# Optimization experiments

Hardware: AMD Instinct MI355X
Metric: run time of the kernel (lower is better)

The kernel has to match this reference:

```python
import jax, jax.numpy as jnp
import numpy as np


def setup_inputs() -> dict:
    key = jax.random.key(0)
    k1, k2, k3, k4, k5 = jax.random.split(key, 5)
    M, K, N, E = 16384, 2048, 5632, 8  # total_tokens, d_model, expert ffn dim, num_experts
    a = jax.random.normal(k1, (M, K), jnp.float32) * 0.1          # fp8-valued activations (simulated in f32)
    b = jax.random.normal(k2, (E, N, K), jnp.float32) * 0.05      # column-major expert weights [E, N, K]
    scale_a = jax.random.uniform(k3, (M, 1), jnp.float32, 0.5, 1.5)   # per-token dequant scale
    scale_b = jax.random.uniform(k4, (E, 1), jnp.float32, 0.5, 1.5)   # per-expert dequant scale
    cuts = jnp.sort(jax.random.randint(k5, (E - 1,), 0, M)).astype(jnp.int32)
    seg_indptr = jnp.concatenate([jnp.zeros(1, jnp.int32), cuts, jnp.full((1,), M, jnp.int32)])
    return {"a": a, "b": b, "scale_a": scale_a, "scale_b": scale_b,
            "seg_indptr": seg_indptr, "batch_size": E}


def reference(a, b, scale_a, scale_b, seg_indptr, batch_size):
    # Grouped GEMM: for expert e, rows seg_indptr[e]:seg_indptr[e+1] of `a` are
    # multiplied by b[e]^T (b is column-major [E, N, K]).
    M = a.shape[0]
    E = b.shape[0]
    group_sizes = jnp.diff(seg_indptr).astype(jnp.int32)           # [E]
    out = jax.lax.ragged_dot(a, jnp.swapaxes(b, 1, 2), group_sizes)  # [M, N]
    # fp8 w8a8 dequant: per-token scale_a, per-expert scale_b gathered per token
    eid = jnp.clip(jnp.searchsorted(seg_indptr, jnp.arange(M), side='right') - 1, 0, E - 1)
    return out * scale_a * scale_b[eid]
```

## Files before the change

kernel.cpp:

```cpp
#include <hip/hip_runtime.h>


#define BK 64
#define NTILES 32
#define BM 256
#define BN 256
#define KDIM 2048

typedef __attribute__((ext_vector_type(4))) float f32x4;
typedef __attribute__((ext_vector_type(4))) unsigned int u32x4;
using frag_ab = __attribute__((ext_vector_type(8))) short;
using frag_cd = __attribute__((ext_vector_type(4))) float;

__device__ __forceinline__ unsigned int pack_bf2(float x, float y) {
  unsigned int ux = __float_as_uint(x);
  unsigned int uy = __float_as_uint(y);
  ux += 0x7fffu + ((ux >> 16) & 1u);
  uy += 0x7fffu + ((uy >> 16) & 1u);
  return (ux >> 16) | (uy & 0xffff0000u);
}

__device__ __forceinline__ void gload_lds16(const void* g, void* lds) {
  __builtin_amdgcn_global_load_lds(
      (const __attribute__((address_space(1))) unsigned int*)g,
      (__attribute__((address_space(3))) unsigned int*)lds, 16, 0, 0);
}

__global__ __launch_bounds__(256)
void convert_kernel(const float* __restrict__ A, const float* __restrict__ B,
                    unsigned short* __restrict__ wa, unsigned short* __restrict__ wb) {
  constexpr long long NA = 16384LL * 2048;
  constexpr long long NB = 8LL * 5632 * 2048;
  constexpr long long NA8 = NA / 8;
  constexpr long long NTOT = (NA + NB) / 8;
  for (long long c = (long long)blockIdx.x * 256 + threadIdx.x; c < NTOT;
       c += (long long)gridDim.x * 256) {
    const float* src;
    unsigned short* dst;
    long long off;
    if (c < NA8) { src = A; dst = wa; off = c * 8; }
    else         { src = B; dst = wb; off = (c - NA8) * 8; }
    f32x4 v0 = *(const f32x4*)(src + off);
    f32x4 v1 = *(const f32x4*)(src + off + 4);
    u32x4 o;
    o[0] = pack_bf2(v0[0], v0[1]);
    o[1] = pack_bf2(v0[2], v0[3]);
    o[2] = pack_bf2(v1[0], v1[1]);
    o[3] = pack_bf2(v1[2], v1[3]);
    *(u32x4*)(dst + off) = o;
  }
}

__global__ __launch_bounds__(512, 2)
void ggemm_q(const unsigned short* __restrict__ A,
             const unsigned short* __restrict__ B,
             const float* __restrict__ sa,
             const float* __restrict__ sb,
             const int* __restrict__ seg,
             float* __restrict__ C) {
  constexpr int M = 16384, N = 5632, E = 8;
  constexpr int NTC = N / BN;
  const int nwg = (M / BM) * NTC;

  int bid = blockIdx.x;
  int sid = (bid & 7) * (nwg >> 3) + (bid >> 3);
  int mt = sid / NTC, nt = sid % NTC;
  int m0 = mt * BM, n0 = nt * BN;

  int tid = threadIdx.x, lane = tid & 63, w = tid >> 6;
  int l16 = lane & 15, lhi = lane >> 4;
  int rw = (w & 1) * 64;
  int cw = (w >> 1) * 32;

  __shared__ unsigned short lds[2][2][2][8192];

  int c7 = l16 & 7;
  int x0 = (lhi ^ c7) * 8;
  int x1 = ((4 | lhi) ^ c7) * 8;
  int offA = (rw + l16) * 64;
  int offB = (cw + l16) * 64;
  int srow = lane >> 3;
  int scol = ((lane & 7) ^ srow) * 8;

  const unsigned short* gA = A + (size_t)(m0 + w * 16 + srow) * KDIM + scol;

  frag_ab af[2][4], bf0[2][2], bf1[2][2];

  for (int e = 0; e < E; ++e) {
    int rlo = max(m0, seg[e]);
    int rhi = min(m0 + BM, seg[e + 1]);
    if (rlo >= rhi) continue;
    const unsigned short* gB =
        B + (size_t)e * N * KDIM + (size_t)(n0 + w * 16 + srow) * KDIM + scol;

    frag_cd acc[4][4][2];
#pragma unroll
    for (int qi = 0; qi < 4; ++qi)
#pragma unroll
      for (int f = 0; f < 4; ++f)
#pragma unroll
        for (int g = 0; g < 2; ++g) acc[qi][f][g] = (frag_cd){0.f, 0.f, 0.f, 0.f};

    auto stA = [&](int buf, int half, int t) {
#pragma unroll
      for (int i = 0; i < 2; ++i)
        gload_lds16(gA + (size_t)(half * 128 + i * 8) * KDIM + t * BK,
                    &lds[buf][0][half][(w * 16 + i * 8) * 64]);
    };
    auto stB = [&](int buf, int half, int t) {
#pragma unroll
      for (int i = 0; i < 2; ++i)
        gload_lds16(gB + (size_t)(half * 128 + i * 8) * KDIM + t * BK,
                    &lds[buf][1][half][(w * 16 + i * 8) * 64]);
    };
    auto rdAf = [&](int buf, int half) {
      const unsigned short* p = &lds[buf][0][half][0];
#pragma unroll
      for (int f = 0; f < 4; ++f) {
        af[0][f] = *(const frag_ab*)(p + offA + f * 1024 + x0);
        af[1][f] = *(const frag_ab*)(p + offA + f * 1024 + x1);
      }
    };
    auto rdBf = [&](int buf, int half, frag_ab (&bf)[2][2]) {
      const unsigned short* p = &lds[buf][1][half][0];
#pragma unroll
      for (int g = 0; g < 2; ++g) {
        bf[0][g] = *(const frag_ab*)(p + offB + g * 1024 + x0);
        bf[1][g] = *(const frag_ab*)(p + offB + g * 1024 + x1);
      }
    };
    auto mfma16 = [&](int qi, frag_ab (&bf)[2][2]) {
      __builtin_amdgcn_s_setprio(1);
#pragma unroll
      for (int f = 0; f < 4; ++f)
#pragma unroll
        for (int g = 0; g < 2; ++g)
#pragma unroll
          for (int ks = 0; ks < 2; ++ks)
            acc[qi][f][g] = __builtin_amdgcn_mfma_f32_16x16x32_bf16(
                af[ks][f], bf[ks][g], acc[qi][f][g], 0, 0, 0);
      __builtin_amdgcn_s_setprio(0);
    };

    stA(0, 0, 0); stB(0, 0, 0); stB(0, 1, 0); stA(0, 1, 0);
    stA(1, 0, 1); stB(1, 0, 1); stB(1, 1, 1); stA(1, 1, 1);
    asm volatile("s_waitcnt vmcnt(8)" ::: "memory");
    __builtin_amdgcn_s_barrier();

    auto tile_body = [&](int t, int buf) {
      bool st = (t + 2 < NTILES);
      rdAf(buf, 0);
      rdBf(buf, 0, bf0);
      __builtin_amdgcn_s_barrier();
      mfma16(0, bf0);
      rdBf(buf, 1, bf1);
      if (st) { stA(buf, 0, t + 2); stB(buf, 0, t + 2); }
      __builtin_amdgcn_s_barrier();
      mfma16(1, bf1);
      rdAf(buf, 1);
      if (st) stB(buf, 1, t + 2);
      __builtin_amdgcn_s_barrier();
      mfma16(2, bf1);
      if (st) stA(buf, 1, t + 2);
      if (t < NTILES - 2) {
        asm volatile("s_waitcnt vmcnt(8)" ::: "memory");
      } else if (t == NTILES - 2) {
        asm volatile("s_waitcnt vmcnt(0)" ::: "memory");
      }
      __builtin_amdgcn_s_barrier();
      mfma16(3, bf0);
    };

    for (int t2 = 0; t2 < NTILES; t2 += 2) {
      tile_body(t2, 0);
      tile_body(t2 + 1, 1);
    }

    const int QMAP[4] = {0, 2, 3, 1};
    float sbe = sb[e];
#pragma unroll
    for (int qi = 0; qi < 4; ++qi) {
      int q = QMAP[qi];
      int rbase = m0 + (q & 1) * 128 + rw;
      int cbase = n0 + (q >> 1) * 128 + cw;
#pragma unroll
      for (int f = 0; f < 4; ++f) {
#pragma unroll
        for (int r = 0; r < 4; ++r) {
          int grow = rbase + f * 16 + lhi * 4 + r;
          if (grow >= rlo && grow < rhi) {
            float s = sa[grow] * sbe;
            float* Crow = C + (size_t)grow * N + cbase;
#pragma unroll
            for (int g = 0; g < 2; ++g)
              Crow[g * 16 + l16] = acc[qi][f][g][r] * s;
          }
        }
      }
    }
  }
}

extern "C" void kernel_launch(void* const* d_in, const int* in_sizes, int n_in,
                              void* d_out, int out_size, void* d_ws, size_t ws_size,
                              hipStream_t stream) {
  const float* a = (const float*)d_in[0];
  const float* b = (const float*)d_in[1];
  const float* sa = (const float*)d_in[2];
  const float* sb = (const float*)d_in[3];
  const int* seg = (const int*)d_in[4];
  float* out = (float*)d_out;

  constexpr size_t NA = 16384ULL * 2048;
  unsigned short* wa = (unsigned short*)d_ws;
  unsigned short* wb = wa + NA;

  hipLaunchKernelGGL(convert_kernel, dim3(2048), dim3(256), 0, stream, a, b, wa, wb);
  hipLaunchKernelGGL(ggemm_q, dim3((16384 / BM) * (5632 / BN)), dim3(512), 0, stream,
                     wa, wb, sa, sb, seg, out);
}
```

Before: 757.6 us.

## Restructure GEMM warp tiling to 128x64 per wave with new LDS pipeline

Changes each wave's output tile from four 64x32 quadrant pieces to one contiguous 128x64 block, holding eight A fragments and four B fragments per k-step. The per-tile schedule is rewritten to split the MFMA work into four 4x2 sub-blocks, interleaved with global-to-LDS prefetches and explicit lgkmcnt/vmcnt waits. The aim is more reuse of A and B fragments read from LDS, fewer LDS reads per MFMA, and a simpler epilogue. In exchange it raises register pressure through larger fragment arrays and adds more barriers, which could hurt occupancy at two workgroups per CU.

```diff
diff --git a/kernel.cpp b/kernel.cpp
--- a/kernel.cpp
+++ b/kernel.cpp
@@ -52,7 +52,7 @@
 }
 
 __global__ __launch_bounds__(512, 2)
-void ggemm_q(const unsigned short* __restrict__ A,
+void ggemm_t(const unsigned short* __restrict__ A,
              const unsigned short* __restrict__ B,
              const float* __restrict__ sa,
              const float* __restrict__ sb,
@@ -69,22 +69,26 @@
 
   int tid = threadIdx.x, lane = tid & 63, w = tid >> 6;
   int l16 = lane & 15, lhi = lane >> 4;
-  int rw = (w & 1) * 64;
-  int cw = (w >> 1) * 32;
-
-  __shared__ unsigned short lds[2][2][2][8192];
+  int wrow = (w >> 2) * 128;
+  int wcol = (w & 3) * 64;
+
+  __shared__ unsigned short Alds[2][256 * 64];
+  __shared__ unsigned short Blds[2][256 * 64];
 
   int c7 = l16 & 7;
-  int x0 = (lhi ^ c7) * 8;
-  int x1 = ((4 | lhi) ^ c7) * 8;
-  int offA = (rw + l16) * 64;
-  int offB = (cw + l16) * 64;
+  int x0 = ((0 + lhi) ^ c7) * 8;
+  int x1 = ((4 + lhi) ^ c7) * 8;
+  int offA[8], offB[4];
+#pragma unroll
+  for (int f = 0; f < 8; ++f) offA[f] = (wrow + f * 16 + l16) * 64;
+#pragma unroll
+  for (int g = 0; g < 4; ++g) offB[g] = (wcol + g * 16 + l16) * 64;
+
   int srow = lane >> 3;
   int scol = ((lane & 7) ^ srow) * 8;
-
   const unsigned short* gA = A + (size_t)(m0 + w * 16 + srow) * KDIM + scol;
 
-  frag_ab af[2][4], bf0[2][2], bf1[2][2];
+  frag_ab af[2][8], bf0[2][2], bf1[2][2];
 
   for (int e = 0; e < E; ++e) {
     int rlo = max(m0, seg[e]);
@@ -93,108 +97,101 @@
     const unsigned short* gB =
         B + (size_t)e * N * KDIM + (size_t)(n0 + w * 16 + srow) * KDIM + scol;
 
-    frag_cd acc[4][4][2];
-#pragma unroll
-    for (int qi = 0; qi < 4; ++qi)
-#pragma unroll
-      for (int f = 0; f < 4; ++f)
-#pragma unroll
-        for (int g = 0; g < 2; ++g) acc[qi][f][g] = (frag_cd){0.f, 0.f, 0.f, 0.f};
-
-    auto stA = [&](int buf, int half, int t) {
+    frag_cd acc[8][4];
+#pragma unroll
+    for (int f = 0; f < 8; ++f)
+#pragma unroll
+      for (int g = 0; g < 4; ++g) acc[f][g] = (frag_cd){0.f, 0.f, 0.f, 0.f};
+
+    auto stA = [&](int b, int h, int t) {
 #pragma unroll
       for (int i = 0; i < 2; ++i)
-        gload_lds16(gA + (size_t)(half * 128 + i * 8) * KDIM + t * BK,
-                    &lds[buf][0][half][(w * 16 + i * 8) * 64]);
-    };
-    auto stB = [&](int buf, int half, int t) {
+        gload_lds16(gA + (size_t)(h * 128 + i * 8) * KDIM + t * BK,
+                    &Alds[b][(h * 128 + w * 16 + i * 8) * 64]);
+    };
+    auto stB = [&](int b, int h, int t) {
 #pragma unroll
       for (int i = 0; i < 2; ++i)
-        gload_lds16(gB + (size_t)(half * 128 + i * 8) * KDIM + t * BK,
-                    &lds[buf][1][half][(w * 16 + i * 8) * 64]);
-    };
-    auto rdAf = [&](int buf, int half) {
-      const unsigned short* p = &lds[buf][0][half][0];
-#pragma unroll
-      for (int f = 0; f < 4; ++f) {
-        af[0][f] = *(const frag_ab*)(p + offA + f * 1024 + x0);
-        af[1][f] = *(const frag_ab*)(p + offA + f * 1024 + x1);
-      }
-    };
-    auto rdBf = [&](int buf, int half, frag_ab (&bf)[2][2]) {
-      const unsigned short* p = &lds[buf][1][half][0];
-#pragma unroll
-      for (int g = 0; g < 2; ++g) {
-        bf[0][g] = *(const frag_ab*)(p + offB + g * 1024 + x0);
-        bf[1][g] = *(const frag_ab*)(p + offB + g * 1024 + x1);
-      }
-    };
-    auto mfma16 = [&](int qi, frag_ab (&bf)[2][2]) {
+        gload_lds16(gB + (size_t)(h * 128 + i * 8) * KDIM + t * BK,
+                    &Blds[b][(h * 128 + w * 16 + i * 8) * 64]);
+    };
+    auto mfma16 = [&](int f0, int g0, frag_ab (&bf)[2][2]) {
       __builtin_amdgcn_s_setprio(1);
 #pragma unroll
-      for (int f = 0; f < 4; ++f)
-#pragma unroll
-        for (int g = 0; g < 2; ++g)
+      for (int fi = 0; fi < 4; ++fi)
+#pragma unroll
+        for (int gi = 0; gi < 2; ++gi)
 #pragma unroll
           for (int ks = 0; ks < 2; ++ks)
-            acc[qi][f][g] = __builtin_amdgcn_mfma_f32_16x16x32_bf16(
-                af[ks][f], bf[ks][g], acc[qi][f][g], 0, 0, 0);
+            acc[f0 + fi][g0 + gi] = __builtin_amdgcn_mfma_f32_16x16x32_bf16(
+                af[ks][f0 + fi], bf[ks][gi], acc[f0 + fi][g0 + gi], 0, 0, 0);
       __builtin_amdgcn_s_setprio(0);
     };
 
-    stA(0, 0, 0); stB(0, 0, 0); stB(0, 1, 0); stA(0, 1, 0);
-    stA(1, 0, 1); stB(1, 0, 1); stB(1, 1, 1); stA(1, 1, 1);
-    asm volatile("s_waitcnt vmcnt(8)" ::: "memory");
+    stA(0, 0, 0); stB(0, 0, 0); stA(0, 1, 0); stB(0, 1, 0);
+    stA(1, 0, 1); stB(1, 0, 1); stA(1, 1, 1);
+    asm volatile("s_waitcnt vmcnt(6)" ::: "memory");
     __builtin_amdgcn_s_barrier();
 
-    auto tile_body = [&](int t, int buf) {
-      bool st = (t + 2 < NTILES);
-      rdAf(buf, 0);
-      rdBf(buf, 0, bf0);
-      __builtin_amdgcn_s_barrier();
-      mfma16(0, bf0);
-      rdBf(buf, 1, bf1);
-      if (st) { stA(buf, 0, t + 2); stB(buf, 0, t + 2); }
-      __builtin_amdgcn_s_barrier();
-      mfma16(1, bf1);
-      rdAf(buf, 1);
-      if (st) stB(buf, 1, t + 2);
-      __builtin_amdgcn_s_barrier();
-      mfma16(2, bf1);
-      if (st) stA(buf, 1, t + 2);
-      if (t < NTILES - 2) {
-        asm volatile("s_waitcnt vmcnt(8)" ::: "memory");
-      } else if (t == NTILES - 2) {
+    auto tile = [&](int t, int b) {
+#pragma unroll
+      for (int f = 0; f < 8; ++f) {
+        af[0][f] = *(const frag_ab*)(&Alds[b][offA[f] + x0]);
+        af[1][f] = *(const frag_ab*)(&Alds[b][offA[f] + x1]);
+      }
+#pragma unroll
+      for (int gi = 0; gi < 2; ++gi) {
+        bf0[0][gi] = *(const frag_ab*)(&Blds[b][offB[gi] + x0]);
+        bf0[1][gi] = *(const frag_ab*)(&Blds[b][offB[gi] + x1]);
+      }
+      if (t + 1 < NTILES) stB(b ^ 1, 1, t + 1);
+      asm volatile("s_waitcnt lgkmcnt(8)" ::: "memory");
+      __builtin_amdgcn_s_barrier();
+      asm volatile("s_waitcnt lgkmcnt(0)" ::: "memory");
+      mfma16(0, 0, bf0);
+      __builtin_amdgcn_s_barrier();
+#pragma unroll
+      for (int gi = 0; gi < 2; ++gi) {
+        bf1[0][gi] = *(const frag_ab*)(&Blds[b][offB[2 + gi] + x0]);
+        bf1[1][gi] = *(const frag_ab*)(&Blds[b][offB[2 + gi] + x1]);
+      }
+      if (t + 2 < NTILES) stA(b, 0, t + 2);
+      __builtin_amdgcn_s_barrier();
+      asm volatile("s_waitcnt lgkmcnt(0)" ::: "memory");
+      mfma16(0, 2, bf1);
+      __builtin_amdgcn_s_barrier();
+      if (t + 2 < NTILES) stB(b, 0, t + 2);
+      __builtin_amdgcn_s_barrier();
+      mfma16(4, 0, bf0);
+      __builtin_amdgcn_s_barrier();
+      if (t + 2 < NTILES) stA(b, 1, t + 2);
+      if (t < NTILES - 3) {
+        asm volatile("s_waitcnt vmcnt(6)" ::: "memory");
+      } else {
         asm volatile("s_waitcnt vmcnt(0)" ::: "memory");
       }
       __builtin_amdgcn_s_barrier();
-      mfma16(3, bf0);
-    };
-
-    for (int t2 = 0; t2 < NTILES; t2 += 2) {
-      tile_body(t2, 0);
-      tile_body(t2 + 1, 1);
+      mfma16(4, 2, bf1);
+      __builtin_amdgcn_s_barrier();
+    };
+
+    for (int tt = 0; tt < NTILES; tt += 2) {
+      tile(tt, 0);
+      tile(tt + 1, 1);
     }
 
-    const int QMAP[4] = {0, 2, 3, 1};
     float sbe = sb[e];
 #pragma unroll
-    for (int qi = 0; qi < 4; ++qi) {
-      int q = QMAP[qi];
-      int rbase = m0 + (q & 1) * 128 + rw;
-      int cbase = n0 + (q >> 1) * 128 + cw;
-#pragma unroll
-      for (int f = 0; f < 4; ++f) {
-#pragma unroll
-        for (int r = 0; r < 4; ++r) {
-          int grow = rbase + f * 16 + lhi * 4 + r;
-          if (grow >= rlo && grow < rhi) {
-            float s = sa[grow] * sbe;
-            float* Crow = C + (size_t)grow * N + cbase;
-#pragma unroll
-            for (int g = 0; g < 2; ++g)
-              Crow[g * 16 + l16] = acc[qi][f][g][r] * s;
-          }
+    for (int f = 0; f < 8; ++f) {
+#pragma unroll
+      for (int r = 0; r < 4; ++r) {
+        int grow = m0 + wrow + f * 16 + lhi * 4 + r;
+        if (grow >= rlo && grow < rhi) {
+          float s = sa[grow] * sbe;
+          float* Crow = C + (size_t)grow * N + n0 + wcol;
+#pragma unroll
+          for (int g = 0; g < 4; ++g)
+            Crow[g * 16 + l16] = acc[f][g][r] * s;
         }
       }
     }
@@ -216,6 +213,6 @@
   unsigned short* wb = wa + NA;
 
   hipLaunchKernelGGL(convert_kernel, dim3(2048), dim3(256), 0, stream, a, b, wa, wb);
-  hipLaunchKernelGGL(ggemm_q, dim3((16384 / BM) * (5632 / BN)), dim3(512), 0, stream,
+  hipLaunchKernelGGL(ggemm_t, dim3((16384 / BM) * (5632 / BN)), dim3(512), 0, stream,
                      wa, wb, sa, sb, seg, out);
 }
```

Measured after the change: 972.9 us. 28.4% more time.
